# Kernel optimization log

Hardware: AMD Instinct MI355X
Metric: run time of the kernel (lower is better)

## Reference

```python
import jax, jax.numpy as jnp
import numpy as np

B, T = 4, 15
NY = NX = 256
RES = 0.05
LAT0 = 32.0
G = 9.81
F0 = 1e-4
C0 = 2.7
DT = 21600.0
TINT = 86400.0
NSTEP = int(TINT // DT)  # 4 Euler sub-steps

# --- grid spacing: mean of dx, dy as in lonlat2dxdy (uniform lon/lat grid) ---
_lat = LAT0 + RES * np.arange(NX, dtype=np.float64)  # lat varies along axis 1
_dx_mean = RES * 111000.0
_dy_mean = RES * 111000.0 * np.mean(np.cos(np.deg2rad(_lat)))
DX = np.float32(0.5 * (_dx_mean + _dy_mean))

# --- Helmholtz operator in DST-I space, shape (NY-2, NX-2) (square grid) ---
_i = np.arange(1, NX - 1, dtype=np.float64)
_j = np.arange(1, NY - 1, dtype=np.float64)
_X, _Y = np.meshgrid(_i, _j, indexing='ij')
_lap = (2 * (np.cos(np.pi / (NX - 1) * _X) - 1) / DX**2
        + 2 * (np.cos(np.pi / (NY - 1) * _Y) - 1) / DX**2)
HELM = jnp.asarray((G / F0) * _lap - G * F0 / C0**2, dtype=jnp.float32)

# --- boundary masks (SSH=None -> no NaN land mask; ind0 is empty) ---
_m = np.full((NY, NX), 3, dtype=np.int32)
_m[0, :] = _m[:, 0] = _m[-1, :] = _m[:, -1] = 1
_m[1, 1:-1] = 2; _m[1:-1, 1] = 2
_m[-2, 1:-1] = 2; _m[-3, 1:-1] = 2
_m[1:-1, -2] = 2; _m[1:-1, -3] = 2
IND12 = jnp.asarray((_m == 1) | (_m == 2))


def dstI1D(x):
    """1D type-I discrete sine transform along last axis."""
    n = x.shape[-1]
    xp = jnp.pad(x, [(0, 0)] * (x.ndim - 1) + [(1, 1)])
    return jnp.fft.irfft(-1j * xp, norm='ortho')[..., 1:n + 1]


def dstI2D(x):
    return jnp.swapaxes(dstI1D(jnp.swapaxes(dstI1D(x), -1, -2)), -1, -2)


def h2uv(h):
    """SSH -> geostrophic (u, v). f is the constant F0."""
    u = jnp.zeros_like(h).at[..., 1:-1, 1:].set(
        -G / F0 * (h[..., 2:, :-1] + h[..., 2:, 1:] - h[..., :-2, 1:] - h[..., :-2, :-1]) / (4 * DX))
    v = jnp.zeros_like(h).at[..., 1:, 1:-1].set(
        G / F0 * (h[..., 1:, 2:] + h[..., :-1, 2:] - h[..., :-1, :-2] - h[..., 1:, :-2]) / (4 * DX))
    return u, v


def h2pv(h, hbc):
    """SSH -> potential vorticity with boundary values from hbc on ind1|ind2."""
    interior = (G / F0 * ((h[..., 2:, 1:-1] + h[..., :-2, 1:-1] - 2 * h[..., 1:-1, 1:-1]) / DX**2
                          + (h[..., 1:-1, 2:] + h[..., 1:-1, :-2] - 2 * h[..., 1:-1, 1:-1]) / DX**2)
                - G * F0 / C0**2 * h[..., 1:-1, 1:-1])
    q = jnp.zeros_like(h).at[..., 1:-1, 1:-1].set(interior)
    return jnp.where(IND12, -G * F0 / C0**2 * hbc, q)


def _adv(up, vp, um, vm, v0):
    """3rd-order upwind advection."""
    c = 1.0 / (6 * DX)
    inner = (
        -up[..., 1:-1, 1:-1] * c * (2 * v0[..., 2:-2, 3:-1] + 3 * v0[..., 2:-2, 2:-2] - 6 * v0[..., 2:-2, 1:-3] + v0[..., 2:-2, :-4])
        + um[..., 1:-1, 1:-1] * c * (v0[..., 2:-2, 4:] - 6 * v0[..., 2:-2, 3:-1] + 3 * v0[..., 2:-2, 2:-2] + 2 * v0[..., 2:-2, 1:-3])
        - vp[..., 1:-1, 1:-1] * c * (2 * v0[..., 3:-1, 2:-2] + 3 * v0[..., 2:-2, 2:-2] - 6 * v0[..., 1:-3, 2:-2] + v0[..., :-4, 2:-2])
        + vm[..., 1:-1, 1:-1] * c * (v0[..., 4:, 2:-2] - 6 * v0[..., 3:-1, 2:-2] + 3 * v0[..., 2:-2, 2:-2] + 2 * v0[..., 1:-3, 2:-2]))
    return jnp.zeros_like(v0).at[..., 2:-2, 2:-2].set(inner)


def rhs(u, v, q0, way=1.0):
    uT = way * 0.5 * (u[..., 1:-1, 1:-1] + u[..., 1:-1, 2:])
    vT = way * 0.5 * (v[..., 1:-1, 1:-1] + v[..., 2:, 1:-1])
    up = jnp.maximum(uT, 0.0); um = jnp.minimum(uT, 0.0)
    vp = jnp.maximum(vT, 0.0); vm = jnp.minimum(vT, 0.0)
    r = _adv(up, vp, um, vm, q0)
    # beta term is identically zero: f = F0 is spatially constant. Kdiffus=None.
    return jnp.where(IND12, 0.0, r)


def pv2h(q, hb, qb):
    """PV -> SSH via DST-based inverse Helmholtz solve."""
    qin = q[..., 1:-1, 1:-1] - qb[..., 1:-1, 1:-1]
    inv = dstI2D(dstI2D(qin) / HELM)
    return jnp.zeros_like(q).at[..., 1:-1, 1:-1].set(inv) + hb


def conv2d(x, w, b):
    y = jax.lax.conv_general_dilated(x, w, (1, 1), 'SAME',
                                     dimension_numbers=('NCHW', 'OIHW', 'NCHW'))
    return y + b[None, :, None, None]


def qg_forecast(x):
    """One-day QG forecast of each frame from the previous one (NSTEP Euler sub-steps)."""
    h0 = x[:, :-1]            # [B, T-1, NY, NX]
    hb = h0                    # background / boundary SSH
    qb = h2pv(hb, hb)

    def body(carry, _):
        h, q = carry
        u, v = h2uv(h)
        q1 = q + DT * rhs(u, v, q)
        h1 = pv2h(q1, hb, qb)
        return (h1, q1), None

    (hf, _), _ = jax.lax.scan(body, (h0, qb), None, length=NSTEP)
    return hf


def setup_inputs() -> dict:
    key = jax.random.key(0)
    ks = jax.random.split(key, 8)
    s = 0.05
    return {
        'x': jax.random.normal(ks[0], (B, T, NY, NX), jnp.float32),
        'w_in': s * jax.random.normal(ks[1], (64, T, 3, 3), jnp.float32),
        'b_in': jnp.zeros((64,), jnp.float32),
        'w_hid': s * jax.random.normal(ks[2], (64, 64, 3, 3), jnp.float32),
        'b_hid': jnp.zeros((64,), jnp.float32),
        'w_b1': s * jax.random.normal(ks[3], (64, 64, 3, 3), jnp.float32),
        'b_b1': jnp.zeros((64,), jnp.float32),
        'w_b21': s * jax.random.normal(ks[4], (64, 64, 3, 3), jnp.float32),
        'b_b21': jnp.zeros((64,), jnp.float32),
        'w_b22': s * jax.random.normal(ks[5], (64, 64, 3, 3), jnp.float32),
        'b_b22': jnp.zeros((64,), jnp.float32),
        'w_out': s * jax.random.normal(ks[6], (T, 128, 3, 3), jnp.float32),
        'b_out': jnp.zeros((T,), jnp.float32),
    }


def reference(x, w_in, b_in, w_hid, b_hid, w_b1, b_b1, w_b21, b_b21,
              w_b22, b_b22, w_out, b_out):
    # QG dynamical prior cost
    hf = qg_forecast(x)
    dyn_cost = jnp.mean((x[:, 1:] - hf) ** 2)
    # bilinear AE prior cost (bilin_quad=False -> product of two branches)
    z = conv2d(x, w_in, b_in)
    z = conv2d(jax.nn.relu(z), w_hid, b_hid)
    nonlin = conv2d(z, w_b21, b_b21) * conv2d(z, w_b22, b_b22)
    xa = conv2d(jnp.concatenate([conv2d(z, w_b1, b_b1), nonlin], axis=1), w_out, b_out)
    ae_cost = jnp.mean((x - xa) ** 2)
    return dyn_cost + ae_cost
```

## Files before the change

kernel.cpp:

```cpp
#include <hip/hip_runtime.h>
#include <math.h>

#define NS 56
#define NPIX 65536

static constexpr double D_PI = 3.14159265358979323846;

typedef __attribute__((ext_vector_type(8))) short short8;
typedef __attribute__((ext_vector_type(4))) float f32x4;
typedef __attribute__((ext_vector_type(16))) float f32x16;

__device__ inline unsigned short f2bf(float f) {
  union { float f; unsigned int u; } v; v.f = f;
  unsigned int r = v.u + 0x7FFFu + ((v.u >> 16) & 1u);
  return (unsigned short)(r >> 16);
}
__device__ inline float bf2f(unsigned short b) {
  union { float f; unsigned int u; } v; v.u = ((unsigned int)b) << 16;
  return v.f;
}

#define SLC      (NS * NPIX)
#define OFF_PART 0
#define OFF_CNT  3584
#define OFF_S    4096
#define OFF_HM   36864
#define OFF_H    102400
#define OFF_QB   (OFF_H + SLC)
#define OFF_DQ0  (OFF_QB + SLC)
#define OFF_DQ1  (OFF_DQ0 + SLC / 2)
#define OFF_A1   (OFF_DQ1 + SLC / 2)
#define OFF_XP   (OFF_A1 + SLC / 2)
#define OFF_Z1   (OFF_XP + 2097152)
#define OFF_Z2   (OFF_Z1 + 8388608)
#define OFF_BC   (OFF_Z2 + 8388608)
#define OFF_XA   (OFF_BC + 8388608)
#define OFF_WT   (OFF_XA + 2097152)
#define W_IN    0
#define W_HID   10240
#define W_B1    47104
#define W_B21   83968
#define W_B22   120832
#define W_O1    157696
#define W_O2    166912

#define QCLAMP 1.0e12f
#define HCLAMP 1.0e15f

__global__ __launch_bounds__(256) void k_preamble(const float* __restrict__ x,
                                                  const float* __restrict__ w_in,
                                                  const float* __restrict__ w_hid,
                                                  const float* __restrict__ w_b1,
                                                  const float* __restrict__ w_b21,
                                                  const float* __restrict__ w_b22,
                                                  const float* __restrict__ w_out,
                                                  unsigned short* __restrict__ S,
                                                  float* __restrict__ HM,
                                                  unsigned short* __restrict__ wtb,
                                                  float* __restrict__ h,
                                                  float* __restrict__ qb,
                                                  unsigned short* __restrict__ xp,
                                                  unsigned int* __restrict__ cnt,
                                                  double* __restrict__ part,
                                                  float dx2, float gf, float gfc) {
  const int blk = blockIdx.x;
  const int tid = threadIdx.x;
  if (blk < 256) {
    int idx = blk * 256 + tid;
    if (idx == 0) *cnt = 0u;
    int i = idx >> 8, j = idx & 255;
    float sv = 0.f, hv = 1.f;
    if (i < 254 && j < 254) {
      double arg = D_PI * (double)((i + 1) * (j + 1)) / 255.0;
      sv = (float)((2.0 / sqrt(510.0)) * sin(arg));
      double la = 2.0 * (cos(D_PI * (double)(i + 1) / 255.0) - 1.0) / (double)dx2
                + 2.0 * (cos(D_PI * (double)(j + 1) / 255.0) - 1.0) / (double)dx2;
      hv = (float)((9.81 / 1e-4) * la - 9.81 * 1e-4 / (2.7 * 2.7));
    }
    S[idx] = f2bf(sv);
    HM[idx] = hv;
  } else if (blk < 256 + 1008) {
    int jb = blk - 256;
    int job = jb / 144;
    int e = (jb - job * 144) * 256 + tid;
    const float* src;
    int dstOff, chunks, icpShift, icw, ic0, icReal, ocw, ocReal;
    switch (job) {
      case 0: src = w_in;  dstOff = W_IN;  chunks = 5;  icpShift = 4; icw = 15;  ic0 = 0;  icReal = 15; ocw = 64; ocReal = 64; break;
      case 1: src = w_hid; dstOff = W_HID; chunks = 18; icpShift = 6; icw = 64;  ic0 = 0;  icReal = 64; ocw = 64; ocReal = 64; break;
      case 2: src = w_b1;  dstOff = W_B1;  chunks = 18; icpShift = 6; icw = 64;  ic0 = 0;  icReal = 64; ocw = 64; ocReal = 64; break;
      case 3: src = w_b21; dstOff = W_B21; chunks = 18; icpShift = 6; icw = 64;  ic0 = 0;  icReal = 64; ocw = 64; ocReal = 64; break;
      case 4: src = w_b22; dstOff = W_B22; chunks = 18; icpShift = 6; icw = 64;  ic0 = 0;  icReal = 64; ocw = 64; ocReal = 64; break;
      case 5: src = w_out; dstOff = W_O1;  chunks = 18; icpShift = 6; icw = 128; ic0 = 0;  icReal = 64; ocw = 16; ocReal = 15; break;
      default: src = w_out; dstOff = W_O2; chunks = 18; icpShift = 6; icw = 128; ic0 = 64; icReal = 64; ocw = 16; ocReal = 15; break;
    }
    int total = chunks * 4 * ocw * 8;
    if (e < total) {
      int j = e & 7;
      int oc = (e >> 3) % ocw;
      int ckg = e / (8 * ocw);
      int kg = ckg & 3, c = ckg >> 2;
      int Kidx = c * 32 + kg * 8 + j;
      int tap = Kidx >> icpShift;
      int ic = Kidx & ((1 << icpShift) - 1);
      float v = 0.f;
      if (tap < 9 && ic < icReal && oc < ocReal)
        v = src[((size_t)oc * icw + ic0 + ic) * 9 + tap];
      wtb[dstOff + e] = f2bf(v);
    }
  } else if (blk < 256 + 1008 + 14336) {
    int idx = (blk - 1264) * 256 + tid;
    int s = idx >> 16, p = idx & 65535;
    int y = p >> 8, xx = p & 255;
    int b = s / 14, t = s - b * 14;
    const float* hb = x + (size_t)(b * 15 + t) * NPIX;
    float hc = hb[p];
    float qv;
    if (y >= 2 && y <= 252 && xx >= 2 && xx <= 252) {
      qv = gf * ((hb[p + 256] + hb[p - 256] - 2.f * hc) / dx2
               + (hb[p + 1] + hb[p - 1] - 2.f * hc) / dx2) - gfc * hc;
    } else {
      qv = -gfc * hc;
    }
    h[idx] = hc;
    qb[idx] = qv;
  } else if (blk < 256 + 1008 + 14336 + 1024) {
    int e = (blk - 15600) * 256 + tid;
    int b = e >> 16, p = e & 65535;
    const float* xb = x + (size_t)b * 15 * NPIX + p;
    union { unsigned short u16[16]; uint4 u4[2]; } vv;
#pragma unroll
    for (int c = 0; c < 15; ++c) vv.u16[c] = f2bf(xb[(size_t)c * NPIX]);
    vv.u16[15] = 0;
    uint4* dst = (uint4*)&xp[(size_t)e * 16];
    dst[0] = vv.u4[0];
    dst[1] = vv.u4[1];
  } else {
    int s = blk - 16624;
    int b = s / 14, t = s - b * 14;
    const float* hb = x + (size_t)(b * 15 + t) * NPIX;
    const float* x1 = x + (size_t)(b * 15 + t + 1) * NPIX;
    double sum = 0.0;
    for (int i = tid; i < 1020; i += 256) {
      int y, xc;
      if (i < 256)      { y = 0;         xc = i; }
      else if (i < 512) { y = 255;       xc = i - 256; }
      else if (i < 766) { y = i - 511;   xc = 0; }
      else              { y = i - 765;   xc = 255; }
      int p = y * 256 + xc;
      float d = x1[p] - hb[p];
      sum += (double)d * (double)d;
    }
    for (int o = 32; o > 0; o >>= 1) sum += __shfl_down(sum, o);
    __shared__ double sw[4];
    int lane = tid & 63, wid = tid >> 6;
    if (lane == 0) sw[wid] = sum;
    __syncthreads();
    if (tid == 0) part[1472 + s] = sw[0] + sw[1] + sw[2] + sw[3];
  }
}

template <bool FIRST>
__global__ __launch_bounds__(256) void k_qrhs_dq(const float* __restrict__ h,
                                                 const float* __restrict__ qbb,
                                                 const unsigned short* __restrict__ dqin,
                                                 unsigned short* __restrict__ dqout,
                                                 float ngf, float pgf, float fdx,
                                                 float cc, float dtf) {
  int idx = blockIdx.x * 256 + threadIdx.x;
  int s = idx >> 16, p = idx & 65535;
  int y = p >> 8, xx = p & 255;
  const float* H = h + (size_t)s * NPIX;
  const float* QB = qbb + (size_t)s * NPIX;
  const unsigned short* DQ = dqin + (size_t)s * NPIX;
  const int base = p - 257;
  auto dqv = [&](int d) -> float {
    if (FIRST) return 0.f;
    return bf2f(DQ[(base + d) & 65535]);
  };
  float q1mqb = 0.f;
  if (y >= 2 && y <= 252 && xx >= 2 && xx <= 252) {
    float hSW = H[p + 255], hS = H[p + 256], hSE = H[p + 257];
    float hNW = H[p - 257], hN = H[p - 256], hNE = H[p - 255];
    float hW = H[p - 1], hE = H[p + 1];
    float uA = ngf * (hSW + hS - hN - hNW) / fdx;
    float uB = ngf * (hS + hSE - hNE - hN) / fdx;
    float vA = pgf * (hE + hNE - hNW - hW) / fdx;
    float vB = pgf * (hSE + hE - hW - hSW) / fdx;
    float uT = 0.5f * (uA + uB);
    float vT = 0.5f * (vA + vB);
    float up = fmaxf(uT, 0.f), um = fminf(uT, 0.f);
    float vp = fmaxf(vT, 0.f), vm = fminf(vT, 0.f);
    float qbc = QB[p];
    float Q0 = qbc + dqv(0);
    float QE = QB[p + 1] + dqv(1), QW = QB[p - 1] + dqv(-1);
    float QEE = QB[p + 2] + dqv(2), QWW = QB[p - 2] + dqv(-2);
    float QS = QB[p + 256] + dqv(256), QN = QB[p - 256] + dqv(-256);
    float QSS = QB[p + 512] + dqv(512), QNN = QB[p - 512] + dqv(-512);
    float r = -up * cc * (2.f * QE + 3.f * Q0 - 6.f * QW + QWW)
            + um * cc * (QEE - 6.f * QE + 3.f * Q0 + 2.f * QW)
            - vp * cc * (2.f * QS + 3.f * Q0 - 6.f * QN + QNN)
            + vm * cc * (QSS - 6.f * QS + 3.f * Q0 + 2.f * QN);
    float q1 = Q0 + dtf * r;
    q1 = fminf(fmaxf(q1, -QCLAMP), QCLAMP);
    q1mqb = q1 - qbc;
  }
  int wy = (y == 0) ? 254 : ((y == 255) ? 255 : y - 1);
  int wx = (xx == 0) ? 254 : ((xx == 255) ? 255 : xx - 1);
  dqout[(size_t)s * NPIX + wy * 256 + wx] = f2bf(q1mqb);
}

template <int EPI>
__global__ __launch_bounds__(512) void k_solve(const unsigned short* __restrict__ Sm,
                                               const unsigned short* __restrict__ Xb,
                                               unsigned short* __restrict__ Ob,
                                               const float* __restrict__ HM,
                                               const float* __restrict__ xin,
                                               float* __restrict__ hout,
                                               double* __restrict__ part) {
  __shared__ unsigned short Ul[32 * 256];
  const int s = blockIdx.x, q = blockIdx.y;
  const unsigned short* X = Xb + (size_t)s * NPIX;
  const int lane = threadIdx.x & 63, w = threadIdx.x >> 6;
  const int r31 = lane & 31, kh = lane >> 5;

  f32x16 acc;
#pragma unroll
  for (int i = 0; i < 16; ++i) acc[i] = 0.f;
  {
    const int ar = (32 * q + r31) * 256;
    const int br = (32 * w + r31) * 256;
#pragma unroll 4
    for (int kc = 0; kc < 256; kc += 16) {
      short8 a = *(const short8*)&Sm[ar + kc + kh * 8];
      short8 b = *(const short8*)&X[br + kc + kh * 8];
      acc = __builtin_amdgcn_mfma_f32_32x32x16_bf16(a, b, acc, 0, 0, 0);
    }
  }
  {
    const int col = 32 * w + r31;
    const int g = col >> 3, c7 = col & 7;
#pragma unroll
    for (int reg = 0; reg < 16; ++reg) {
      int i = (reg & 3) + 8 * (reg >> 2) + 4 * kh;
      Ul[i * 256 + (((g ^ (i & 7)) << 3) | c7)] = f2bf(acc[reg]);
    }
  }
  __syncthreads();

  f32x16 acc2;
#pragma unroll
  for (int i = 0; i < 16; ++i) acc2[i] = 0.f;
  {
    const int ar = (32 * w + r31) * 256;
    const int urow = r31 * 256;
    const int x7 = (r31 & 7);
#pragma unroll 4
    for (int kc = 0; kc < 256; kc += 16) {
      int g0 = (kc >> 3) + kh;
      short8 a = *(const short8*)&Sm[ar + kc + kh * 8];
      short8 b = *(const short8*)&Ul[urow + ((g0 ^ x7) << 3)];
      acc2 = __builtin_amdgcn_mfma_f32_32x32x16_bf16(a, b, acc2, 0, 0, 0);
    }
  }
  const int gn = 32 * q + r31;
  if (EPI == 0) {
    unsigned short* O = Ob + (size_t)s * NPIX;
#pragma unroll
    for (int reg = 0; reg < 16; ++reg) {
      int gm = 32 * w + (reg & 3) + 8 * (reg >> 2) + 4 * kh;
      O[(size_t)gm * 256 + gn] = f2bf(acc2[reg] / HM[(size_t)gm * 256 + gn]);
    }
  } else if (EPI == 1) {
    int b = s / 14, t = s - b * 14;
    const float* hb = xin + (size_t)(b * 15 + t) * NPIX;
    float* H = hout + (size_t)s * NPIX;
    if (gn < 254) {
#pragma unroll
      for (int reg = 0; reg < 16; ++reg) {
        int gm = 32 * w + (reg & 3) + 8 * (reg >> 2) + 4 * kh;
        if (gm < 254) {
          size_t o = (size_t)(gm + 1) * 256 + (gn + 1);
          float hv = acc2[reg] + hb[o];
          H[o] = fminf(fmaxf(hv, -HCLAMP), HCLAMP);
        }
      }
    }
  } else {
    int b = s / 14, t = s - b * 14;
    const float* hb = xin + (size_t)(b * 15 + t) * NPIX;
    const float* x1 = xin + (size_t)(b * 15 + t + 1) * NPIX;
    double dsum = 0.0;
    if (gn < 254) {
#pragma unroll
      for (int reg = 0; reg < 16; ++reg) {
        int gm = 32 * w + (reg & 3) + 8 * (reg >> 2) + 4 * kh;
        if (gm < 254) {
          size_t o = (size_t)(gm + 1) * 256 + (gn + 1);
          float hv = acc2[reg] + hb[o];
          hv = fminf(fmaxf(hv, -HCLAMP), HCLAMP);
          float d = x1[o] - hv;
          dsum += (double)d * (double)d;
        }
      }
    }
    for (int o = 32; o > 0; o >>= 1) dsum += __shfl_down(dsum, o);
    __shared__ double sred[8];
    if (lane == 0) sred[w] = dsum;
    __syncthreads();
    if (threadIdx.x == 0) {
      double t8 = 0.0;
#pragma unroll
      for (int i = 0; i < 8; ++i) t8 += sred[i];
      part[1024 + s * 8 + q] = t8;
    }
  }
}

template <bool RELU, int EMODE>
__global__ __launch_bounds__(512) void k_conv64b(const unsigned short* __restrict__ in,
                                                 const unsigned short* __restrict__ wt,
                                                 const float* __restrict__ bias,
                                                 const unsigned short* __restrict__ other,
                                                 unsigned short* __restrict__ out) {
  __shared__ unsigned short tile[324 * 64];
  const int tid = threadIdx.x;
  const int lane = tid & 63, wave = tid >> 6;
  const int cl = lane & 15, kg = lane >> 4;
  const int wrow = wave & 3, wh = wave >> 2;
  const int b = blockIdx.z;
  const int gx0 = blockIdx.x * 16, gy0 = blockIdx.y * 16;

  f32x4 acc[4][2];
#pragma unroll
  for (int j = 0; j < 2; ++j) {
    float bv = bias[wh * 32 + j * 16 + cl];
#pragma unroll
    for (int i = 0; i < 4; ++i) acc[i][j] = (f32x4){bv, bv, bv, bv};
  }

  const unsigned short* inb = in + (size_t)b * NPIX * 64;
  for (int c = tid; c < 2592; c += 512) {
    int pp = c >> 3, g = c & 7;
    int ly = pp / 18, lx = pp - ly * 18;
    int iy = gy0 + ly - 1, ix = gx0 + lx - 1;
    uint4 v = make_uint4(0u, 0u, 0u, 0u);
    if (iy >= 0 && iy < 256 && ix >= 0 && ix < 256)
      v = *(const uint4*)&inb[((size_t)iy * 256 + ix) * 64 + g * 8];
    int sw = g ^ (pp & 7);
    *(uint4*)&tile[pp * 64 + sw * 8] = v;
  }
  __syncthreads();

#pragma unroll 3
  for (int cm = 0; cm < 18; ++cm) {
    const int tap = cm >> 1;
    const int g = (cm & 1) * 4 + kg;
    const int dy = tap / 3, dxx = tap - dy * 3;
    short8 bfr[2];
#pragma unroll
    for (int j = 0; j < 2; ++j)
      bfr[j] = *(const short8*)&wt[(((size_t)cm * 4 + kg) * 64 + wh * 32 + j * 16 + cl) * 8];
    const int tc = cl + dxx;
#pragma unroll
    for (int i = 0; i < 4; ++i) {
      int pp = (wrow * 4 + i + dy) * 18 + tc;
      int g2 = g ^ (pp & 7);
      short8 av = *(const short8*)&tile[pp * 64 + g2 * 8];
#pragma unroll
      for (int j = 0; j < 2; ++j)
        acc[i][j] = __builtin_amdgcn_mfma_f32_16x16x32_bf16(av, bfr[j], acc[i][j], 0, 0, 0);
    }
  }

  const size_t outBase = (size_t)b * NPIX * 64;
#pragma unroll
  for (int i = 0; i < 4; ++i) {
    int y = gy0 + wrow * 4 + i;
#pragma unroll
    for (int j = 0; j < 2; ++j) {
      int oc = wh * 32 + j * 16 + cl;
#pragma unroll
      for (int r = 0; r < 4; ++r) {
        int px = gx0 + kg * 4 + r;
        size_t oi = outBase + ((size_t)y * 256 + px) * 64 + oc;
        float v = acc[i][j][r];
        if (EMODE == 1) v *= bf2f(other[oi]);
        if (RELU) v = fmaxf(v, 0.f);
        out[oi] = f2bf(v);
      }
    }
  }
}

__global__ __launch_bounds__(512) void k_convmul(const unsigned short* __restrict__ in,
                                                 const unsigned short* __restrict__ wtA,
                                                 const unsigned short* __restrict__ wtB,
                                                 const float* __restrict__ biasA,
                                                 const float* __restrict__ biasB,
                                                 unsigned short* __restrict__ out) {
  __shared__ unsigned short tile[324 * 64];
  const int tid = threadIdx.x;
  const int lane = tid & 63, wave = tid >> 6;
  const int cl = lane & 15, kg = lane >> 4;
  const int wrow = wave & 3, wh = wave >> 2;
  const int b = blockIdx.z;
  const int gx0 = blockIdx.x * 16, gy0 = blockIdx.y * 16;

  f32x4 accA[4][2], accB[4][2];
#pragma unroll
  for (int j = 0; j < 2; ++j) {
    float ba = biasA[wh * 32 + j * 16 + cl], bb = biasB[wh * 32 + j * 16 + cl];
#pragma unroll
    for (int i = 0; i < 4; ++i) {
      accA[i][j] = (f32x4){ba, ba, ba, ba};
      accB[i][j] = (f32x4){bb, bb, bb, bb};
    }
  }

  const unsigned short* inb = in + (size_t)b * NPIX * 64;
  for (int c = tid; c < 2592; c += 512) {
    int pp = c >> 3, g = c & 7;
    int ly = pp / 18, lx = pp - ly * 18;
    int iy = gy0 + ly - 1, ix = gx0 + lx - 1;
    uint4 v = make_uint4(0u, 0u, 0u, 0u);
    if (iy >= 0 && iy < 256 && ix >= 0 && ix < 256)
      v = *(const uint4*)&inb[((size_t)iy * 256 + ix) * 64 + g * 8];
    int sw = g ^ (pp & 7);
    *(uint4*)&tile[pp * 64 + sw * 8] = v;
  }
  __syncthreads();

#pragma unroll 2
  for (int cm = 0; cm < 18; ++cm) {
    const int tap = cm >> 1;
    const int g = (cm & 1) * 4 + kg;
    const int dy = tap / 3, dxx = tap - dy * 3;
    const int tc = cl + dxx;
    short8 wa[2], wb[2];
#pragma unroll
    for (int j = 0; j < 2; ++j) {
      wa[j] = *(const short8*)&wtA[(((size_t)cm * 4 + kg) * 64 + wh * 32 + j * 16 + cl) * 8];
      wb[j] = *(const short8*)&wtB[(((size_t)cm * 4 + kg) * 64 + wh * 32 + j * 16 + cl) * 8];
    }
#pragma unroll
    for (int i = 0; i < 4; ++i) {
      int pp = (wrow * 4 + i + dy) * 18 + tc;
      int g2 = g ^ (pp & 7);
      short8 av = *(const short8*)&tile[pp * 64 + g2 * 8];
#pragma unroll
      for (int j = 0; j < 2; ++j) {
        accA[i][j] = __builtin_amdgcn_mfma_f32_16x16x32_bf16(av, wa[j], accA[i][j], 0, 0, 0);
        accB[i][j] = __builtin_amdgcn_mfma_f32_16x16x32_bf16(av, wb[j], accB[i][j], 0, 0, 0);
      }
    }
  }

  const size_t outBase = (size_t)b * NPIX * 64;
#pragma unroll
  for (int i = 0; i < 4; ++i) {
    int y = gy0 + wrow * 4 + i;
#pragma unroll
    for (int j = 0; j < 2; ++j) {
      int oc = wh * 32 + j * 16 + cl;
#pragma unroll
      for (int r = 0; r < 4; ++r) {
        int px = gx0 + kg * 4 + r;
        size_t oi = outBase + ((size_t)y * 256 + px) * 64 + oc;
        out[oi] = f2bf(accA[i][j][r] * accB[i][j][r]);
      }
    }
  }
}

__global__ __launch_bounds__(512) void k_convout(const unsigned short* __restrict__ in0,
                                                 const unsigned short* __restrict__ in1,
                                                 const unsigned short* __restrict__ wt,
                                                 const float* __restrict__ bias,
                                                 unsigned short* __restrict__ out) {
  __shared__ unsigned short tile[324 * 64];
  const int tid = threadIdx.x;
  const int lane = tid & 63, wave = tid >> 6;
  const int cl = lane & 15, kg = lane >> 4;
  const int b = blockIdx.z;
  const int gx0 = blockIdx.x * 16, gy0 = blockIdx.y * 16;

  f32x4 acc[2];
  {
    float bv = (cl < 15) ? bias[cl] : 0.f;
    acc[0] = (f32x4){bv, bv, bv, bv};
    acc[1] = acc[0];
  }

  for (int src = 0; src < 2; ++src) {
    const unsigned short* inb = (src ? in1 : in0) + (size_t)b * NPIX * 64;
    const unsigned short* wtp = wt + src * 9216;
    if (src) __syncthreads();
    for (int c = tid; c < 2592; c += 512) {
      int pp = c >> 3, g = c & 7;
      int ly = pp / 18, lx = pp - ly * 18;
      int iy = gy0 + ly - 1, ix = gx0 + lx - 1;
      uint4 v = make_uint4(0u, 0u, 0u, 0u);
      if (iy >= 0 && iy < 256 && ix >= 0 && ix < 256)
        v = *(const uint4*)&inb[((size_t)iy * 256 + ix) * 64 + g * 8];
      int sw = g ^ (pp & 7);
      *(uint4*)&tile[pp * 64 + sw * 8] = v;
    }
    __syncthreads();
#pragma unroll 3
    for (int cm = 0; cm < 18; ++cm) {
      const int tap = cm >> 1;
      const int g = (cm & 1) * 4 + kg;
      const int dy = tap / 3, dxx = tap - dy * 3;
      short8 bfr = *(const short8*)&wtp[(((size_t)cm * 4 + kg) * 16 + cl) * 8];
      const int tc = cl + dxx;
#pragma unroll
      for (int i = 0; i < 2; ++i) {
        int pp = (wave * 2 + i + dy) * 18 + tc;
        int g2 = g ^ (pp & 7);
        short8 av = *(const short8*)&tile[pp * 64 + g2 * 8];
        acc[i] = __builtin_amdgcn_mfma_f32_16x16x32_bf16(av, bfr, acc[i], 0, 0, 0);
      }
    }
  }

  const size_t outBase = (size_t)b * NPIX * 16;
#pragma unroll
  for (int i = 0; i < 2; ++i) {
    int y = gy0 + wave * 2 + i;
#pragma unroll
    for (int r = 0; r < 4; ++r) {
      int px = gx0 + kg * 4 + r;
      size_t oi = outBase + ((size_t)y * 256 + px) * 16 + cl;
      out[oi] = f2bf(acc[i][r]);
    }
  }
}

__global__ __launch_bounds__(256) void k_conv16(const unsigned short* __restrict__ in,
                                                const unsigned short* __restrict__ wt,
                                                const float* __restrict__ bias,
                                                unsigned short* __restrict__ out) {
  __shared__ unsigned short wlds[10240];
  __shared__ unsigned short tile[324 * 16];

  const int tid = threadIdx.x;
  const int lane = tid & 63, wave = tid >> 6;
  const int cl = lane & 15, kg = lane >> 4;
  const int b = blockIdx.z;
  const int gx0 = blockIdx.x * 16, gy0 = blockIdx.y * 16;

  {
    uint4* wl = (uint4*)wlds;
    const uint4* wg = (const uint4*)wt;
    for (int i = tid; i < 1280; i += 256) wl[i] = wg[i];
  }
  const unsigned short* inb = in + (size_t)b * NPIX * 16;
  for (int c = tid; c < 648; c += 256) {
    int pp = c >> 1, g = c & 1;
    int ly = pp / 18, lx = pp - ly * 18;
    int iy = gy0 + ly - 1, ix = gx0 + lx - 1;
    uint4 v = make_uint4(0u, 0u, 0u, 0u);
    if (iy >= 0 && iy < 256 && ix >= 0 && ix < 256)
      v = *(const uint4*)&inb[((size_t)iy * 256 + ix) * 16 + g * 8];
    int sw = g ^ (pp & 1);
    *(uint4*)&tile[pp * 16 + sw * 8] = v;
  }
  __syncthreads();

  f32x4 acc[4][4];
#pragma unroll
  for (int j = 0; j < 4; ++j) {
    float bv = bias[j * 16 + cl];
#pragma unroll
    for (int i = 0; i < 4; ++i) acc[i][j] = (f32x4){bv, bv, bv, bv};
  }

#pragma unroll
  for (int c = 0; c < 5; ++c) {
    int tap = 2 * c + (kg >> 1);
    int dy = tap / 3, dxx = tap - dy * 3;
    int gidx = kg & 1;
    short8 bfr[4];
#pragma unroll
    for (int j = 0; j < 4; ++j)
      bfr[j] = *(const short8*)&wlds[((c * 4 + kg) * 64 + j * 16 + cl) * 8];
    int tc = cl + dxx;
#pragma unroll
    for (int i = 0; i < 4; ++i) {
      int tr = wave * 4 + i + dy;
      if (tr > 17) tr = 17;
      int pp = tr * 18 + tc;
      int g2 = gidx ^ (pp & 1);
      short8 av = *(const short8*)&tile[pp * 16 + g2 * 8];
#pragma unroll
      for (int j = 0; j < 4; ++j)
        acc[i][j] = __builtin_amdgcn_mfma_f32_16x16x32_bf16(av, bfr[j], acc[i][j], 0, 0, 0);
    }
  }

  const size_t outBase = (size_t)b * NPIX * 64;
#pragma unroll
  for (int i = 0; i < 4; ++i) {
    int y = gy0 + wave * 4 + i;
#pragma unroll
    for (int j = 0; j < 4; ++j) {
      int oc = j * 16 + cl;
#pragma unroll
      for (int r = 0; r < 4; ++r) {
        int px = gx0 + kg * 4 + r;
        size_t oi = outBase + ((size_t)y * 256 + px) * 64 + oc;
        out[oi] = f2bf(fmaxf(acc[i][j][r], 0.f));
      }
    }
  }
}

__global__ __launch_bounds__(256) void k_red_ae(const float* __restrict__ x,
                                                const unsigned short* __restrict__ xa,
                                                double* __restrict__ part,
                                                unsigned int* __restrict__ cnt,
                                                float* __restrict__ out) {
  const int NBT = 1024;
  const int bid = blockIdx.x;
  const int tid = threadIdx.x;
  const int e = bid * 256 + tid;
  const int b = e >> 16, p = e & 65535;
  union { unsigned short u16[16]; uint4 u4[2]; } vv;
  const uint4* xap = (const uint4*)&xa[(size_t)e * 16];
  vv.u4[0] = xap[0];
  vv.u4[1] = xap[1];
  const float* xb = x + (size_t)b * 15 * NPIX + p;
  double sum = 0.0;
#pragma unroll
  for (int c = 0; c < 15; ++c) {
    float d = xb[(size_t)c * NPIX] - bf2f(vv.u16[c]);
    sum += (double)d * (double)d;
  }
  for (int o = 32; o > 0; o >>= 1) sum += __shfl_down(sum, o);
  __shared__ double sw[4];
  __shared__ bool last;
  int lane = tid & 63, wid = tid >> 6;
  if (lane == 0) sw[wid] = sum;
  __syncthreads();
  if (tid == 0) {
    part[bid] = sw[0] + sw[1] + sw[2] + sw[3];
    __threadfence();
    unsigned int t = atomicAdd(cnt, 1u);
    last = (t == (unsigned)(NBT - 1));
  }
  __syncthreads();
  if (last) {
    __threadfence();
    double s1 = 0.0, s2 = 0.0;
    for (int i = tid; i < 504; i += 256) s1 += part[1024 + i];
    for (int i = tid; i < NBT; i += 256) s2 += part[i];
    for (int o = 32; o > 0; o >>= 1) {
      s1 += __shfl_down(s1, o);
      s2 += __shfl_down(s2, o);
    }
    __shared__ double a1[4], a2[4];
    if (lane == 0) { a1[wid] = s1; a2[wid] = s2; }
    __syncthreads();
    if (tid == 0) {
      double v = (a1[0] + a1[1] + a1[2] + a1[3]) / (double)(NS * NPIX)
               + (a2[0] + a2[1] + a2[2] + a2[3]) / (double)(60 * NPIX);
      if (!(v == v)) v = 0.0;
      if (v > 1.0e30) v = 1.0e30;
      if (v < -1.0e30) v = -1.0e30;
      out[0] = (float)v;
    }
  }
}

extern "C" void kernel_launch(void* const* d_in, const int* in_sizes, int n_in,
                              void* d_out, int out_size, void* d_ws, size_t ws_size,
                              hipStream_t stream) {
  (void)in_sizes; (void)n_in; (void)out_size; (void)ws_size;
  const float* x     = (const float*)d_in[0];
  const float* w_in  = (const float*)d_in[1];
  const float* b_in  = (const float*)d_in[2];
  const float* w_hid = (const float*)d_in[3];
  const float* b_hid = (const float*)d_in[4];
  const float* w_b1  = (const float*)d_in[5];
  const float* b_b1  = (const float*)d_in[6];
  const float* w_b21 = (const float*)d_in[7];
  const float* b_b21 = (const float*)d_in[8];
  const float* w_b22 = (const float*)d_in[9];
  const float* b_b22 = (const float*)d_in[10];
  const float* w_out = (const float*)d_in[11];
  const float* b_out = (const float*)d_in[12];
  float* ws = (float*)d_ws;
  float* out = (float*)d_out;

  double mc = 0.0;
  for (int k = 0; k < 256; ++k) mc += cos((32.0 + 0.05 * k) * D_PI / 180.0);
  mc /= 256.0;
  float DXf = (float)(0.5 * (5550.0 + 5550.0 * mc));
  float dx2 = DXf * DXf;
  float gf  = (float)(9.81 / 1e-4);
  float ngf = (float)(-9.81 / 1e-4);
  float gfc = (float)(9.81 * 1e-4 / (2.7 * 2.7));
  float fdx = 4.0f * DXf;
  float cc  = 1.0f / (6.0f * DXf);
  float dtf = 21600.0f;

  double* part = (double*)d_ws;
  unsigned int* cnt = (unsigned int*)(ws + OFF_CNT);
  unsigned short* S  = (unsigned short*)(ws + OFF_S);
  float* HM = ws + OFF_HM;
  float* h  = ws + OFF_H;
  float* qb = ws + OFF_QB;
  unsigned short* dq0 = (unsigned short*)(ws + OFF_DQ0);
  unsigned short* dq1 = (unsigned short*)(ws + OFF_DQ1);
  unsigned short* A1 = (unsigned short*)(ws + OFF_A1);
  unsigned short* xp = (unsigned short*)(ws + OFF_XP);
  unsigned short* z1 = (unsigned short*)(ws + OFF_Z1);
  unsigned short* z2 = (unsigned short*)(ws + OFF_Z2);
  unsigned short* bc = (unsigned short*)(ws + OFF_BC);
  unsigned short* xa = (unsigned short*)(ws + OFF_XA);
  unsigned short* wtb = (unsigned short*)(ws + OFF_WT);

  k_preamble<<<dim3(16680), dim3(256), 0, stream>>>(x, w_in, w_hid, w_b1, w_b21, w_b22,
                                                    w_out, S, HM, wtb, h, qb, xp, cnt,
                                                    part, dx2, gf, gfc);

  dim3 sg(56, 8);
  dim3 qg(NS * NPIX / 256);
  unsigned short* dqc = dq0;
  unsigned short* dqn = dq1;
  for (int step = 0; step < 4; ++step) {
    if (step == 0)
      k_qrhs_dq<true><<<qg, dim3(256), 0, stream>>>(h, qb, dq1, dqc, ngf, gf, fdx, cc, dtf);
    else {
      k_qrhs_dq<false><<<qg, dim3(256), 0, stream>>>(h, qb, dqc, dqn, ngf, gf, fdx, cc, dtf);
      unsigned short* tmp = dqc; dqc = dqn; dqn = tmp;
    }
    k_solve<0><<<sg, dim3(512), 0, stream>>>(S, dqc, A1, HM, nullptr, nullptr, part);
    if (step < 3)
      k_solve<1><<<sg, dim3(512), 0, stream>>>(S, A1, nullptr, nullptr, x, h, part);
    else
      k_solve<2><<<sg, dim3(512), 0, stream>>>(S, A1, nullptr, nullptr, x, nullptr, part);
  }

  dim3 cg4(16, 16, 4);
  k_conv16<<<cg4, dim3(256), 0, stream>>>(xp, wtb + W_IN, b_in, z1);
  k_conv64b<false, 0><<<cg4, dim3(512), 0, stream>>>(z1, wtb + W_HID, b_hid, nullptr, z2);
  k_conv64b<false, 0><<<cg4, dim3(512), 0, stream>>>(z2, wtb + W_B1, b_b1, nullptr, z1);
  k_convmul<<<cg4, dim3(512), 0, stream>>>(z2, wtb + W_B21, wtb + W_B22, b_b21, b_b22, bc);
  k_convout<<<cg4, dim3(512), 0, stream>>>(z1, bc, wtb + W_O1, b_out, xa);

  k_red_ae<<<dim3(1024), dim3(256), 0, stream>>>(x, xa, part, cnt, out);
}
```

Measured before the change: 488.4 us.

## Fuse QG forecast steps into one cooperative persistent kernel with grid syncs

Replaces the 12 per-step launches (qrhs plus two spectral solve kernels per step) with one cooperative kernel of 448 blocks that runs all four Euler steps and uses grid.sync between phases. The aim is to remove kernel launch gaps and tail effects between the small dependent kernels. A fallback path keeps the old launches if cooperative launch or occupancy is insufficient. Grid-wide barriers carry their own cost, and the fused kernel may use more registers and reach lower occupancy.

```diff
diff --git a/kernel.cpp b/kernel.cpp
--- a/kernel.cpp
+++ b/kernel.cpp
@@ -1,5 +1,8 @@
 #include <hip/hip_runtime.h>
+#include <hip/hip_cooperative_groups.h>
 #include <math.h>
+
+namespace cg = cooperative_groups;
 
 #define NS 56
 #define NPIX 65536
@@ -210,20 +213,10 @@
   dqout[(size_t)s * NPIX + wy * 256 + wx] = f2bf(q1mqb);
 }
 
-template <int EPI>
-__global__ __launch_bounds__(512) void k_solve(const unsigned short* __restrict__ Sm,
-                                               const unsigned short* __restrict__ Xb,
-                                               unsigned short* __restrict__ Ob,
-                                               const float* __restrict__ HM,
-                                               const float* __restrict__ xin,
-                                               float* __restrict__ hout,
-                                               double* __restrict__ part) {
-  __shared__ unsigned short Ul[32 * 256];
-  const int s = blockIdx.x, q = blockIdx.y;
-  const unsigned short* X = Xb + (size_t)s * NPIX;
-  const int lane = threadIdx.x & 63, w = threadIdx.x >> 6;
-  const int r31 = lane & 31, kh = lane >> 5;
-
+__device__ inline f32x16 solve_core(const unsigned short* __restrict__ Sm,
+                                    const unsigned short* __restrict__ X,
+                                    unsigned short* __restrict__ Ul,
+                                    int q, int w, int r31, int kh) {
   f32x16 acc;
 #pragma unroll
   for (int i = 0; i < 16; ++i) acc[i] = 0.f;
@@ -247,7 +240,6 @@
     }
   }
   __syncthreads();
-
   f32x16 acc2;
 #pragma unroll
   for (int i = 0; i < 16; ++i) acc2[i] = 0.f;
@@ -263,6 +255,22 @@
       acc2 = __builtin_amdgcn_mfma_f32_32x32x16_bf16(a, b, acc2, 0, 0, 0);
     }
   }
+  return acc2;
+}
+
+template <int EPI>
+__global__ __launch_bounds__(512) void k_solve(const unsigned short* __restrict__ Sm,
+                                               const unsigned short* __restrict__ Xb,
+                                               unsigned short* __restrict__ Ob,
+                                               const float* __restrict__ HM,
+                                               const float* __restrict__ xin,
+                                               float* __restrict__ hout,
+                                               double* __restrict__ part) {
+  __shared__ unsigned short Ul[32 * 256];
+  const int s = blockIdx.x, q = blockIdx.y;
+  const int lane = threadIdx.x & 63, w = threadIdx.x >> 6;
+  const int r31 = lane & 31, kh = lane >> 5;
+  f32x16 acc2 = solve_core(Sm, Xb + (size_t)s * NPIX, Ul, q, w, r31, kh);
   const int gn = 32 * q + r31;
   if (EPI == 0) {
     unsigned short* O = Ob + (size_t)s * NPIX;
@@ -313,6 +321,146 @@
 #pragma unroll
       for (int i = 0; i < 8; ++i) t8 += sred[i];
       part[1024 + s * 8 + q] = t8;
+    }
+  }
+}
+
+__global__ __launch_bounds__(512, 4) void k_qg_coop(const unsigned short* __restrict__ Sm,
+                                                    const float* __restrict__ x,
+                                                    float* __restrict__ h,
+                                                    const float* __restrict__ qb,
+                                                    unsigned short* __restrict__ dq0,
+                                                    unsigned short* __restrict__ dq1,
+                                                    unsigned short* __restrict__ A1,
+                                                    const float* __restrict__ HM,
+                                                    double* __restrict__ part,
+                                                    float ngf, float pgf, float fdx,
+                                                    float cc, float dtf) {
+  cg::grid_group grid = cg::this_grid();
+  __shared__ unsigned short Ul[32 * 256];
+  const int tid = threadIdx.x;
+  const int bid = blockIdx.x;
+  const int s = bid >> 3, q = bid & 7;
+  const int lane = tid & 63, w = tid >> 6;
+  const int r31 = lane & 31, kh = lane >> 5;
+
+  for (int step = 0; step < 4; ++step) {
+    const unsigned short* rd = (step & 1) ? dq0 : dq1;
+    unsigned short* wr = (step & 1) ? dq1 : dq0;
+    for (int it = 0; it < 16; ++it) {
+      int idx = it * 229376 + bid * 512 + tid;
+      int s2 = idx >> 16, p = idx & 65535;
+      int y = p >> 8, xx = p & 255;
+      const float* H = h + (size_t)s2 * NPIX;
+      const float* QB = qb + (size_t)s2 * NPIX;
+      const unsigned short* DQ = rd + (size_t)s2 * NPIX;
+      const int base = p - 257;
+      float q1mqb = 0.f;
+      if (y >= 2 && y <= 252 && xx >= 2 && xx <= 252) {
+        float hSW = H[p + 255], hS = H[p + 256], hSE = H[p + 257];
+        float hNW = H[p - 257], hN = H[p - 256], hNE = H[p - 255];
+        float hW = H[p - 1], hE = H[p + 1];
+        float uA = ngf * (hSW + hS - hN - hNW) / fdx;
+        float uB = ngf * (hS + hSE - hNE - hN) / fdx;
+        float vA = pgf * (hE + hNE - hNW - hW) / fdx;
+        float vB = pgf * (hSE + hE - hW - hSW) / fdx;
+        float uT = 0.5f * (uA + uB);
+        float vT = 0.5f * (vA + vB);
+        float up = fmaxf(uT, 0.f), um = fminf(uT, 0.f);
+        float vp = fmaxf(vT, 0.f), vm = fminf(vT, 0.f);
+        float qbc = QB[p];
+        float d0 = 0.f, dE = 0.f, dW = 0.f, dEE = 0.f, dWW = 0.f;
+        float dS = 0.f, dN = 0.f, dSS = 0.f, dNN = 0.f;
+        if (step != 0) {
+          d0 = bf2f(DQ[base & 65535]);
+          dE = bf2f(DQ[(base + 1) & 65535]);
+          dW = bf2f(DQ[(base - 1) & 65535]);
+          dEE = bf2f(DQ[(base + 2) & 65535]);
+          dWW = bf2f(DQ[(base - 2) & 65535]);
+          dS = bf2f(DQ[(base + 256) & 65535]);
+          dN = bf2f(DQ[(base - 256) & 65535]);
+          dSS = bf2f(DQ[(base + 512) & 65535]);
+          dNN = bf2f(DQ[(base - 512) & 65535]);
+        }
+        float Q0 = qbc + d0;
+        float QE = QB[p + 1] + dE, QW = QB[p - 1] + dW;
+        float QEE = QB[p + 2] + dEE, QWW = QB[p - 2] + dWW;
+        float QS = QB[p + 256] + dS, QN = QB[p - 256] + dN;
+        float QSS = QB[p + 512] + dSS, QNN = QB[p - 512] + dNN;
+        float r = -up * cc * (2.f * QE + 3.f * Q0 - 6.f * QW + QWW)
+                + um * cc * (QEE - 6.f * QE + 3.f * Q0 + 2.f * QW)
+                - vp * cc * (2.f * QS + 3.f * Q0 - 6.f * QN + QNN)
+                + vm * cc * (QSS - 6.f * QS + 3.f * Q0 + 2.f * QN);
+        float q1 = Q0 + dtf * r;
+        q1 = fminf(fmaxf(q1, -QCLAMP), QCLAMP);
+        q1mqb = q1 - qbc;
+      }
+      int wy = (y == 0) ? 254 : ((y == 255) ? 255 : y - 1);
+      int wx = (xx == 0) ? 254 : ((xx == 255) ? 255 : xx - 1);
+      wr[(size_t)s2 * NPIX + wy * 256 + wx] = f2bf(q1mqb);
+    }
+    grid.sync();
+    {
+      f32x16 acc2 = solve_core(Sm, wr + (size_t)s * NPIX, Ul, q, w, r31, kh);
+      const int gn = 32 * q + r31;
+      unsigned short* O = A1 + (size_t)s * NPIX;
+#pragma unroll
+      for (int reg = 0; reg < 16; ++reg) {
+        int gm = 32 * w + (reg & 3) + 8 * (reg >> 2) + 4 * kh;
+        O[(size_t)gm * 256 + gn] = f2bf(acc2[reg] / HM[(size_t)gm * 256 + gn]);
+      }
+    }
+    grid.sync();
+    __syncthreads();
+    {
+      f32x16 acc2 = solve_core(Sm, A1 + (size_t)s * NPIX, Ul, q, w, r31, kh);
+      const int gn = 32 * q + r31;
+      int b = s / 14, t = s - b * 14;
+      const float* hb = x + (size_t)(b * 15 + t) * NPIX;
+      if (step < 3) {
+        float* H = h + (size_t)s * NPIX;
+        if (gn < 254) {
+#pragma unroll
+          for (int reg = 0; reg < 16; ++reg) {
+            int gm = 32 * w + (reg & 3) + 8 * (reg >> 2) + 4 * kh;
+            if (gm < 254) {
+              size_t o = (size_t)(gm + 1) * 256 + (gn + 1);
+              float hv = acc2[reg] + hb[o];
+              H[o] = fminf(fmaxf(hv, -HCLAMP), HCLAMP);
+            }
+          }
+        }
+      } else {
+        const float* x1 = x + (size_t)(b * 15 + t + 1) * NPIX;
+        double dsum = 0.0;
+        if (gn < 254) {
+#pragma unroll
+          for (int reg = 0; reg < 16; ++reg) {
+            int gm = 32 * w + (reg & 3) + 8 * (reg >> 2) + 4 * kh;
+            if (gm < 254) {
+              size_t o = (size_t)(gm + 1) * 256 + (gn + 1);
+              float hv = acc2[reg] + hb[o];
+              hv = fminf(fmaxf(hv, -HCLAMP), HCLAMP);
+              float d = x1[o] - hv;
+              dsum += (double)d * (double)d;
+            }
+          }
+        }
+        for (int o = 32; o > 0; o >>= 1) dsum += __shfl_down(dsum, o);
+        __shared__ double sred[8];
+        if (lane == 0) sred[w] = dsum;
+        __syncthreads();
+        if (tid == 0) {
+          double t8 = 0.0;
+#pragma unroll
+          for (int i = 0; i < 8; ++i) t8 += sred[i];
+          part[1024 + bid] = t8;
+        }
+      }
+    }
+    if (step < 3) {
+      grid.sync();
+      __syncthreads();
     }
   }
 }
@@ -725,22 +873,43 @@
                                                     w_out, S, HM, wtb, h, qb, xp, cnt,
                                                     part, dx2, gf, gfc);
 
-  dim3 sg(56, 8);
-  dim3 qg(NS * NPIX / 256);
-  unsigned short* dqc = dq0;
-  unsigned short* dqn = dq1;
-  for (int step = 0; step < 4; ++step) {
-    if (step == 0)
-      k_qrhs_dq<true><<<qg, dim3(256), 0, stream>>>(h, qb, dq1, dqc, ngf, gf, fdx, cc, dtf);
-    else {
-      k_qrhs_dq<false><<<qg, dim3(256), 0, stream>>>(h, qb, dqc, dqn, ngf, gf, fdx, cc, dtf);
-      unsigned short* tmp = dqc; dqc = dqn; dqn = tmp;
-    }
-    k_solve<0><<<sg, dim3(512), 0, stream>>>(S, dqc, A1, HM, nullptr, nullptr, part);
-    if (step < 3)
-      k_solve<1><<<sg, dim3(512), 0, stream>>>(S, A1, nullptr, nullptr, x, h, part);
-    else
-      k_solve<2><<<sg, dim3(512), 0, stream>>>(S, A1, nullptr, nullptr, x, nullptr, part);
+  bool coopOK = false;
+  {
+    int maxBlocks = 0;
+    hipError_t oe = hipOccupancyMaxActiveBlocksPerMultiprocessor(
+        &maxBlocks, (const void*)k_qg_coop, 512, 0);
+    if (oe == hipSuccess && maxBlocks >= 2) {
+      const unsigned short* Sc = S;
+      const float* xc = x;
+      const float* qbc2 = qb;
+      const float* HMc = HM;
+      void* args[] = {(void*)&Sc, (void*)&xc, (void*)&h, (void*)&qbc2,
+                      (void*)&dq0, (void*)&dq1, (void*)&A1, (void*)&HMc,
+                      (void*)&part, (void*)&ngf, (void*)&gf, (void*)&fdx,
+                      (void*)&cc, (void*)&dtf};
+      hipError_t le = hipLaunchCooperativeKernel((void*)k_qg_coop, dim3(448), dim3(512),
+                                                 args, 0, stream);
+      coopOK = (le == hipSuccess);
+    }
+  }
+  if (!coopOK) {
+    dim3 sg(56, 8);
+    dim3 qg(NS * NPIX / 256);
+    unsigned short* dqc = dq0;
+    unsigned short* dqn = dq1;
+    for (int step = 0; step < 4; ++step) {
+      if (step == 0)
+        k_qrhs_dq<true><<<qg, dim3(256), 0, stream>>>(h, qb, dq1, dqc, ngf, gf, fdx, cc, dtf);
+      else {
+        k_qrhs_dq<false><<<qg, dim3(256), 0, stream>>>(h, qb, dqc, dqn, ngf, gf, fdx, cc, dtf);
+        unsigned short* tmp = dqc; dqc = dqn; dqn = tmp;
+      }
+      k_solve<0><<<sg, dim3(512), 0, stream>>>(S, dqc, A1, HM, nullptr, nullptr, part);
+      if (step < 3)
+        k_solve<1><<<sg, dim3(512), 0, stream>>>(S, A1, nullptr, nullptr, x, h, part);
+      else
+        k_solve<2><<<sg, dim3(512), 0, stream>>>(S, A1, nullptr, nullptr, x, nullptr, part);
+    }
   }
 
   dim3 cg4(16, 16, 4);
```

Measured after the change: 487.5 us. Within noise of the previous version (-0.2%).
